# Kernel optimization log

Hardware: AMD Instinct MI355X
Metric: run time of the kernel (lower is better)

Reference implementation:

```python
import jax, jax.numpy as jnp
import numpy as np

VOCAB = 128

def setup_inputs() -> dict:
    key = jax.random.key(0)
    k1, k2, k3, k4 = jax.random.split(key, 4)
    B, S, H = 64, 512, 1024
    x = jax.random.randint(k1, (B, S), 0, VOCAB, dtype=jnp.int32)
    h = jnp.zeros((B, H), dtype=jnp.float32)
    # Xavier-normal-ish scaled params
    W_xh = jax.random.normal(k2, (VOCAB, H), dtype=jnp.float32) * (2.0 / (VOCAB + H)) ** 0.5
    W_hh = jax.random.normal(k3, (H, H), dtype=jnp.float32) * (1.0 / H) ** 0.5
    b_h = jnp.zeros((H,), dtype=jnp.float32)
    W_out = jax.random.normal(k4, (H, VOCAB), dtype=jnp.float32) * (1.0 / H) ** 0.5
    b_out = jnp.zeros((VOCAB,), dtype=jnp.float32)
    return {"x": x, "h": h, "W_xh": W_xh, "W_hh": W_hh, "b_h": b_h,
            "W_out": W_out, "b_out": b_out}

def reference(x, h, W_xh, W_hh, b_h, W_out, b_out):
    """x: (B,S) int32, h: (B,H). Returns (logits (B,S,V), h_final (B,H)).
    one_hot(x) @ W_xh == embedding gather W_xh[x] (same math, no dense one-hot).
    Dropout is identity (eval mode). Sequential tanh recurrence via lax.scan."""
    x_emb = W_xh[x]                      # (B, S, H) gather == one-hot matmul
    x_emb_t = jnp.swapaxes(x_emb, 0, 1)  # (S, B, H) scan over time

    def step(h, xe):
        h_new = jnp.tanh(xe + h @ W_hh + b_h)
        return h_new, h_new

    h_final, hidden = jax.lax.scan(step, h, x_emb_t)  # hidden: (S, B, H)
    hidden = jnp.swapaxes(hidden, 0, 1)               # (B, S, H)
    logits = hidden @ W_out + b_out                   # (B, S, V)
    return logits, h_final
```

## Files before the change

kernel.cpp:

```cpp
#include <hip/hip_runtime.h>
#include <hip/hip_bf16.h>
#include <stdint.h>


#define Bz 64
#define Sz 512
#define Hz 1024
#define Vz 128
#define NWG 32
#define COLS 32
#define WGT 512

typedef __attribute__((ext_vector_type(8)))  short short8;
typedef __attribute__((ext_vector_type(16))) float f32x16;
typedef __attribute__((ext_vector_type(4)))  unsigned u32x4;
typedef __attribute__((ext_vector_type(2)))  unsigned u32x2;

__device__ __align__(16) unsigned short g_hfrag[3][2][64][64][8];
__device__ __align__(16) unsigned short g_hidden[(size_t)Sz*2*64*64*8];
__device__ __align__(16) unsigned short g_wout[64*4*64*8];

__device__ __forceinline__ unsigned short f2bf(float f) {
  union { float f; unsigned u; } v; v.f = f;
  unsigned r = v.u + 0x7FFFu + ((v.u >> 16) & 1u);
  return (unsigned short)(r >> 16);
}

__device__ __forceinline__ float fast_tanh(float x) {
  float cx = fminf(9.0f, fmaxf(-9.0f, x));
  float e  = __builtin_amdgcn_exp2f(cx * 2.88539008178f);
  return (e - 1.0f) * __builtin_amdgcn_rcpf(e + 1.0f);
}

__device__ __forceinline__ void load_afrags16(const unsigned short* p0, u32x4 t[16]) {
  const unsigned short* p1 = p0 + 2048;
  const unsigned short* p2 = p0 + 4096;
  const unsigned short* p3 = p0 + 6144;
  asm volatile(
    "global_load_dwordx4 %0,  %16, off sc1\n\t"
    "global_load_dwordx4 %1,  %16, off offset:1024 sc1\n\t"
    "global_load_dwordx4 %2,  %16, off offset:2048 sc1\n\t"
    "global_load_dwordx4 %3,  %16, off offset:3072 sc1\n\t"
    "global_load_dwordx4 %4,  %17, off sc1\n\t"
    "global_load_dwordx4 %5,  %17, off offset:1024 sc1\n\t"
    "global_load_dwordx4 %6,  %17, off offset:2048 sc1\n\t"
    "global_load_dwordx4 %7,  %17, off offset:3072 sc1\n\t"
    "global_load_dwordx4 %8,  %18, off sc1\n\t"
    "global_load_dwordx4 %9,  %18, off offset:1024 sc1\n\t"
    "global_load_dwordx4 %10, %18, off offset:2048 sc1\n\t"
    "global_load_dwordx4 %11, %18, off offset:3072 sc1\n\t"
    "global_load_dwordx4 %12, %19, off sc1\n\t"
    "global_load_dwordx4 %13, %19, off offset:1024 sc1\n\t"
    "global_load_dwordx4 %14, %19, off offset:2048 sc1\n\t"
    "global_load_dwordx4 %15, %19, off offset:3072 sc1\n\t"
    "s_waitcnt vmcnt(0)"
    : "=&v"(t[0]), "=&v"(t[1]), "=&v"(t[2]),  "=&v"(t[3]),
      "=&v"(t[4]), "=&v"(t[5]), "=&v"(t[6]),  "=&v"(t[7]),
      "=&v"(t[8]), "=&v"(t[9]), "=&v"(t[10]), "=&v"(t[11]),
      "=&v"(t[12]),"=&v"(t[13]),"=&v"(t[14]), "=&v"(t[15])
    : "v"(p0), "v"(p1), "v"(p2), "v"(p3)
    : "memory");
}

__device__ __forceinline__ void store16_sc1(unsigned short* p, u32x4 v) {
  asm volatile("global_store_dwordx4 %0, %1, off sc1" :: "v"(p), "v"(v) : "memory");
}
__device__ __forceinline__ void store8_sc1(unsigned short* p, u32x2 v) {
  asm volatile("global_store_dwordx2 %0, %1, off sc1" :: "v"(p), "v"(v) : "memory");
}

__global__ void pack_wout(const float* __restrict__ W_out) {
  int gid = blockIdx.x * blockDim.x + threadIdx.x;
  int lane = gid & 63;
  int nt   = (gid >> 6) & 3;
  int kb   = gid >> 8;
  int n = nt * 32 + (lane & 31);
  int k0 = kb * 16 + (lane >> 5) * 8;
  unsigned short t[8];
#pragma unroll
  for (int j = 0; j < 8; ++j)
    t[j] = f2bf(W_out[(size_t)(k0 + j) * Vz + n]);
  uint4 w;
  w.x = (unsigned)t[0] | ((unsigned)t[1] << 16);
  w.y = (unsigned)t[2] | ((unsigned)t[3] << 16);
  w.z = (unsigned)t[4] | ((unsigned)t[5] << 16);
  w.w = (unsigned)t[6] | ((unsigned)t[7] << 16);
  *(uint4*)&g_wout[(size_t)gid * 8] = w;
}

__global__ __launch_bounds__(WGT) void rnn_persistent(
    const int* __restrict__ x, const float* __restrict__ h0,
    const float* __restrict__ W_xh, const float* __restrict__ W_hh,
    const float* __restrict__ b_h, float* __restrict__ out,
    unsigned* __restrict__ flags)
{
  __shared__ unsigned short ldsW[128 * 32 * 8];
  __shared__ float red[4 * 64 * 32];

  const int g    = blockIdx.x;
  const int n0g  = g * COLS;
  const int tid  = threadIdx.x;
  const int lane = tid & 63;
  const int wv   = tid >> 6;
  const int mi   = wv & 1;
  const int ki   = wv >> 1;
  const int bn   = lane & 31;

  for (int idx = tid; idx < 128 * 32; idx += WGT) {
    int kb = idx >> 5, n = idx & 31;
    unsigned short t[8];
#pragma unroll
    for (int j = 0; j < 8; ++j)
      t[j] = f2bf(W_hh[(size_t)(kb * 8 + j) * Hz + n0g + n]);
    uint4 w;
    w.x = (unsigned)t[0] | ((unsigned)t[1] << 16);
    w.y = (unsigned)t[2] | ((unsigned)t[3] << 16);
    w.z = (unsigned)t[4] | ((unsigned)t[5] << 16);
    w.w = (unsigned)t[6] | ((unsigned)t[7] << 16);
    *(uint4*)&ldsW[(size_t)idx * 8] = w;
  }

  if (tid < 256) {
    int s_idx = g * 256 + tid;
    int fmi = s_idx >> 12, fkb = (s_idx >> 6) & 63, fL = s_idx & 63;
    int m = fmi * 32 + (fL & 31);
    int k = fkb * 16 + (fL >> 5) * 8;
    const float* src = &h0[(size_t)m * Hz + k];
    float4 a0 = *(const float4*)&src[0];
    float4 a1 = *(const float4*)&src[4];
    u32x4 w;
    w.x = (unsigned)f2bf(a0.x) | ((unsigned)f2bf(a0.y) << 16);
    w.y = (unsigned)f2bf(a0.z) | ((unsigned)f2bf(a0.w) << 16);
    w.z = (unsigned)f2bf(a1.x) | ((unsigned)f2bf(a1.y) << 16);
    w.w = (unsigned)f2bf(a1.z) | ((unsigned)f2bf(a1.w) << 16);
    store16_sc1(&g_hfrag[0][fmi][fkb][fL][0], w);
  }

  {
    __syncthreads();
    if (tid == 0)
      __hip_atomic_store(&flags[g * 8], 1u, __ATOMIC_RELAXED,
                         __HIP_MEMORY_SCOPE_AGENT);
    if (wv == 0) {
      for (int it = 0; it < 65536; ++it) {
        unsigned v = 0xFFFFFFFFu;
        if (lane < NWG)
          v = __hip_atomic_load(&flags[lane * 8], __ATOMIC_RELAXED,
                                __HIP_MEMORY_SCOPE_AGENT);
        if (__all(v >= 1u)) break;
        __builtin_amdgcn_s_sleep(1);
      }
    }
    __syncthreads();
    asm volatile("" ::: "memory");
  }

  const int em   = (lane & 31) + 32 * (wv & 1);
  const int c0   = ((wv >> 1) * 2 + (lane >> 5)) * 4;
  const int kcol = n0g + c0;
  const int kb_g = kcol >> 4;
  const int kq   = (c0 >> 3) & 1;
  const int lslot = kq * 32 + (em & 31);
  const size_t slotOff =
      ((((size_t)(wv & 1) * 64 + kb_g) * 64) + lslot) * 8 + (c0 & 7);
  float bias[4];
#pragma unroll
  for (int j = 0; j < 4; ++j) bias[j] = b_h[kcol + j];

  const int pflag = (8 * ki + (lane & 7)) * 8;

  int tok_n = x[em * Sz];
  float4 xv_n = *(const float4*)&W_xh[(size_t)tok_n * Hz + kcol];

  int rp = 0;
  for (int s = 0; s < Sz; ++s) {
    const int wp = (rp == 2) ? 0 : rp + 1;

    u32x4 t[16];
    load_afrags16(&g_hfrag[rp][mi][ki * 16][lane][0], t);
    short8 a[16];
#pragma unroll
    for (int kst = 0; kst < 16; ++kst) a[kst] = *(short8*)&t[kst];

    f32x16 acc = {};
#pragma unroll
    for (int kst = 0; kst < 16; ++kst) {
      int kb8 = ki * 32 + kst * 2 + (lane >> 5);
      short8 b = *(const short8*)&ldsW[(size_t)(kb8 * 32 + bn) * 8];
      acc = __builtin_amdgcn_mfma_f32_32x32x16_bf16(a[kst], b, acc, 0, 0, 0);
    }

    float4 xv = xv_n;
    if (s + 1 < Sz) {
      int t2 = x[em * Sz + s + 1];
      xv_n = *(const float4*)&W_xh[(size_t)t2 * Hz + kcol];
    }

    {
      const int crow = 4 * (lane >> 5);
      float* reg = &red[ki * 2048];
#pragma unroll
      for (int r = 0; r < 16; ++r) {
        int m = mi * 32 + crow + (r & 3) + 8 * (r >> 2);
        reg[m * 32 + (bn ^ (m & 31))] = acc[r];
      }
    }
    __syncthreads();

    float z[4];
    {
      const int sw = em & 31;
      const int base = em * 32;
#pragma unroll
      for (int j = 0; j < 4; ++j) {
        int off = base + ((c0 + j) ^ sw);
        z[j] = (red[off] + red[2048 + off]) + (red[4096 + off] + red[6144 + off]);
      }
    }
    z[0] = fast_tanh(z[0] + xv.x + bias[0]);
    z[1] = fast_tanh(z[1] + xv.y + bias[1]);
    z[2] = fast_tanh(z[2] + xv.z + bias[2]);
    z[3] = fast_tanh(z[3] + xv.w + bias[3]);

    u32x2 w2;
    w2.x = (unsigned)f2bf(z[0]) | ((unsigned)f2bf(z[1]) << 16);
    w2.y = (unsigned)f2bf(z[2]) | ((unsigned)f2bf(z[3]) << 16);

    store8_sc1(&((unsigned short*)g_hfrag)[(size_t)wp * 65536 + slotOff], w2);

    if (s == Sz - 1) {
      *(u32x2*)&g_hidden[(size_t)s * 65536 + slotOff] = w2;
      float* hf = out + (size_t)Bz * Sz * Vz + (size_t)em * Hz + kcol;
      float4 f0 = {z[0], z[1], z[2], z[3]};
      *(float4*)hf = f0;
    } else {
      __syncthreads();
      if (tid == 0)
        __hip_atomic_store(&flags[g * 8], (unsigned)(s + 2), __ATOMIC_RELAXED,
                           __HIP_MEMORY_SCOPE_AGENT);
      *(u32x2*)&g_hidden[(size_t)s * 65536 + slotOff] = w2;
      {
        const unsigned tgt = (unsigned)(s + 2);
        for (int it = 0; it < 65536; ++it) {
          unsigned v = 0xFFFFFFFFu;
          if (lane < 8)
            v = __hip_atomic_load(&flags[pflag], __ATOMIC_RELAXED,
                                  __HIP_MEMORY_SCOPE_AGENT);
          if (__all(v >= tgt)) break;
          __builtin_amdgcn_s_sleep(1);
        }
      }
      asm volatile("" ::: "memory");
    }
    rp = wp;
  }
}

__global__ __launch_bounds__(256) void logits_gemm(
    const float* __restrict__ b_out, float* __restrict__ out)
{
  const int tid = threadIdx.x, lane = tid & 63, nt = tid >> 6;
  const int s = blockIdx.x >> 1, mi = blockIdx.x & 1;
  const unsigned short* ab = &g_hidden[((size_t)s * 8192 + (size_t)mi * 4096) * 8];

  f32x16 acc = {};
#pragma unroll 8
  for (int kb = 0; kb < 64; ++kb) {
    short8 a = *(const short8*)&ab[(size_t)(kb * 64 + lane) * 8];
    short8 b = *(const short8*)&g_wout[(size_t)((kb * 4 + nt) * 64 + lane) * 8];
    acc = __builtin_amdgcn_mfma_f32_32x32x16_bf16(a, b, acc, 0, 0, 0);
  }
  const int col = nt * 32 + (lane & 31);
  const float bo = b_out[col];
  const int rbase = 4 * (lane >> 5);
#pragma unroll
  for (int r = 0; r < 16; ++r) {
    int m = rbase + (r & 3) + 8 * (r >> 2);
    int em = mi * 32 + m;
    out[((size_t)em * Sz + s) * Vz + col] = acc[r] + bo;
  }
}

extern "C" void kernel_launch(void* const* d_in, const int* in_sizes, int n_in,
                              void* d_out, int out_size, void* d_ws, size_t ws_size,
                              hipStream_t stream) {
  const int*   x     = (const int*)d_in[0];
  const float* h0    = (const float*)d_in[1];
  const float* W_xh  = (const float*)d_in[2];
  const float* W_hh  = (const float*)d_in[3];
  const float* b_h   = (const float*)d_in[4];
  const float* W_out = (const float*)d_in[5];
  const float* b_out = (const float*)d_in[6];
  float* out = (float*)d_out;

  (void)hipMemsetAsync(d_ws, 0, 1024, stream);
  pack_wout<<<64, 256, 0, stream>>>(W_out);
  rnn_persistent<<<NWG, WGT, 0, stream>>>(x, h0, W_xh, W_hh, b_h, out,
                                          (unsigned*)d_ws);
  logits_gemm<<<Sz * 2, 256, 0, stream>>>(b_out, out);
}
```

Measured before the change: 1.724 ms.

## Replace end-of-step barrier wait with per-producer flag polling pipelined with loads

Removes the all-producers spin wait at the end of each timestep. Each wave now polls one producer workgroup's flag right before loading that producer's slice of the hidden state, then issues the next loads while running MFMAs on data that has already arrived. This lets computation on early-ready chunks overlap with waiting on slower producers and with load latency. In exchange each step makes eight serialized flag polls, and the vmcnt-based waits written in inline asm have to order correctly with the flag check and the triple-buffered state.

Result: slower. 2.483 ms (+44.0%).

```diff
diff --git a/kernel.cpp b/kernel.cpp
--- a/kernel.cpp
+++ b/kernel.cpp
@@ -32,34 +32,20 @@
   return (e - 1.0f) * __builtin_amdgcn_rcpf(e + 1.0f);
 }
 
-__device__ __forceinline__ void load_afrags16(const unsigned short* p0, u32x4 t[16]) {
-  const unsigned short* p1 = p0 + 2048;
-  const unsigned short* p2 = p0 + 4096;
-  const unsigned short* p3 = p0 + 6144;
+__device__ __forceinline__ void load2_sc1(const unsigned short* p,
+                                          u32x4& t0, u32x4& t1) {
   asm volatile(
-    "global_load_dwordx4 %0,  %16, off sc1\n\t"
-    "global_load_dwordx4 %1,  %16, off offset:1024 sc1\n\t"
-    "global_load_dwordx4 %2,  %16, off offset:2048 sc1\n\t"
-    "global_load_dwordx4 %3,  %16, off offset:3072 sc1\n\t"
-    "global_load_dwordx4 %4,  %17, off sc1\n\t"
-    "global_load_dwordx4 %5,  %17, off offset:1024 sc1\n\t"
-    "global_load_dwordx4 %6,  %17, off offset:2048 sc1\n\t"
-    "global_load_dwordx4 %7,  %17, off offset:3072 sc1\n\t"
-    "global_load_dwordx4 %8,  %18, off sc1\n\t"
-    "global_load_dwordx4 %9,  %18, off offset:1024 sc1\n\t"
-    "global_load_dwordx4 %10, %18, off offset:2048 sc1\n\t"
-    "global_load_dwordx4 %11, %18, off offset:3072 sc1\n\t"
-    "global_load_dwordx4 %12, %19, off sc1\n\t"
-    "global_load_dwordx4 %13, %19, off offset:1024 sc1\n\t"
-    "global_load_dwordx4 %14, %19, off offset:2048 sc1\n\t"
-    "global_load_dwordx4 %15, %19, off offset:3072 sc1\n\t"
-    "s_waitcnt vmcnt(0)"
-    : "=&v"(t[0]), "=&v"(t[1]), "=&v"(t[2]),  "=&v"(t[3]),
-      "=&v"(t[4]), "=&v"(t[5]), "=&v"(t[6]),  "=&v"(t[7]),
-      "=&v"(t[8]), "=&v"(t[9]), "=&v"(t[10]), "=&v"(t[11]),
-      "=&v"(t[12]),"=&v"(t[13]),"=&v"(t[14]), "=&v"(t[15])
-    : "v"(p0), "v"(p1), "v"(p2), "v"(p3)
+    "global_load_dwordx4 %0, %2, off sc1\n\t"
+    "global_load_dwordx4 %1, %2, off offset:1024 sc1"
+    : "=&v"(t0), "=&v"(t1)
+    : "v"(p)
     : "memory");
+}
+__device__ __forceinline__ void waitv2(u32x4& a, u32x4& b) {
+  asm volatile("s_waitcnt vmcnt(2)" : "+v"(a), "+v"(b));
+}
+__device__ __forceinline__ void waitv0(u32x4& a, u32x4& b) {
+  asm volatile("s_waitcnt vmcnt(0)" : "+v"(a), "+v"(b));
 }
 
 __device__ __forceinline__ void store16_sc1(unsigned short* p, u32x4 v) {
@@ -155,6 +141,16 @@
     asm volatile("" ::: "memory");
   }
 
+  auto pollflag = [&](int gp, unsigned tgt) {
+    const unsigned* fp = &flags[gp * 8];
+    for (int it = 0; it < 65536; ++it) {
+      if (__hip_atomic_load(fp, __ATOMIC_RELAXED,
+                            __HIP_MEMORY_SCOPE_AGENT) >= tgt) break;
+      __builtin_amdgcn_s_sleep(1);
+    }
+    asm volatile("" ::: "memory");
+  };
+
   const int em   = (lane & 31) + 32 * (wv & 1);
   const int c0   = ((wv >> 1) * 2 + (lane >> 5)) * 4;
   const int kcol = n0g + c0;
@@ -167,27 +163,41 @@
 #pragma unroll
   for (int j = 0; j < 4; ++j) bias[j] = b_h[kcol + j];
 
-  const int pflag = (8 * ki + (lane & 7)) * 8;
-
   int tok_n = x[em * Sz];
   float4 xv_n = *(const float4*)&W_xh[(size_t)tok_n * Hz + kcol];
 
   int rp = 0;
   for (int s = 0; s < Sz; ++s) {
     const int wp = (rp == 2) ? 0 : rp + 1;
-
+    const unsigned tgt = (unsigned)(s + 1);
+
+    const unsigned short* pb = &g_hfrag[rp][mi][ki * 16][lane][0];
     u32x4 t[16];
-    load_afrags16(&g_hfrag[rp][mi][ki * 16][lane][0], t);
-    short8 a[16];
-#pragma unroll
-    for (int kst = 0; kst < 16; ++kst) a[kst] = *(short8*)&t[kst];
-
     f32x16 acc = {};
-#pragma unroll
-    for (int kst = 0; kst < 16; ++kst) {
-      int kb8 = ki * 32 + kst * 2 + (lane >> 5);
-      short8 b = *(const short8*)&ldsW[(size_t)(kb8 * 32 + bn) * 8];
-      acc = __builtin_amdgcn_mfma_f32_32x32x16_bf16(a[kst], b, acc, 0, 0, 0);
+    pollflag(8 * ki + 0, tgt);
+    load2_sc1(pb, t[0], t[1]);
+#pragma unroll
+    for (int j = 0; j < 7; ++j) {
+      pollflag(8 * ki + j + 1, tgt);
+      load2_sc1(pb + (size_t)(j + 1) * 1024, t[2 * j + 2], t[2 * j + 3]);
+      waitv2(t[2 * j], t[2 * j + 1]);
+      {
+        int kb8a = ki * 32 + (2 * j) * 2 + (lane >> 5);
+        int kb8b = ki * 32 + (2 * j + 1) * 2 + (lane >> 5);
+        short8 ba = *(const short8*)&ldsW[(size_t)(kb8a * 32 + bn) * 8];
+        short8 bb = *(const short8*)&ldsW[(size_t)(kb8b * 32 + bn) * 8];
+        acc = __builtin_amdgcn_mfma_f32_32x32x16_bf16(*(short8*)&t[2 * j],     ba, acc, 0, 0, 0);
+        acc = __builtin_amdgcn_mfma_f32_32x32x16_bf16(*(short8*)&t[2 * j + 1], bb, acc, 0, 0, 0);
+      }
+    }
+    waitv0(t[14], t[15]);
+    {
+      int kb8a = ki * 32 + 14 * 2 + (lane >> 5);
+      int kb8b = ki * 32 + 15 * 2 + (lane >> 5);
+      short8 ba = *(const short8*)&ldsW[(size_t)(kb8a * 32 + bn) * 8];
+      short8 bb = *(const short8*)&ldsW[(size_t)(kb8b * 32 + bn) * 8];
+      acc = __builtin_amdgcn_mfma_f32_32x32x16_bf16(*(short8*)&t[14], ba, acc, 0, 0, 0);
+      acc = __builtin_amdgcn_mfma_f32_32x32x16_bf16(*(short8*)&t[15], bb, acc, 0, 0, 0);
     }
 
     float4 xv = xv_n;
@@ -239,17 +249,6 @@
         __hip_atomic_store(&flags[g * 8], (unsigned)(s + 2), __ATOMIC_RELAXED,
                            __HIP_MEMORY_SCOPE_AGENT);
       *(u32x2*)&g_hidden[(size_t)s * 65536 + slotOff] = w2;
-      {
-        const unsigned tgt = (unsigned)(s + 2);
-        for (int it = 0; it < 65536; ++it) {
-          unsigned v = 0xFFFFFFFFu;
-          if (lane < 8)
-            v = __hip_atomic_load(&flags[pflag], __ATOMIC_RELAXED,
-                                  __HIP_MEMORY_SCOPE_AGENT);
-          if (__all(v >= tgt)) break;
-          __builtin_amdgcn_s_sleep(1);
-        }
-      }
       asm volatile("" ::: "memory");
     }
     rp = wp;
```
